# Kernel optimization log

Measured on AMD Instinct MI355X. Metric: run time of the kernel, lower is better.

Reference implementation:

```python
import jax, jax.numpy as jnp
import numpy as np

DIM = 256
NEMB = 1024
NUM = 4
KS = (1, 3, 5, 7)
B, S = 8, 2048


def _conv_same(x, w, b):
    # x: [B,1,S,D], w: [1,1,k,D] -> SAME padding, stride 1 keeps [B,1,S,D]
    y = jax.lax.conv_general_dilated(x, w, window_strides=(1, 1), padding='SAME',
                                     dimension_numbers=('NCHW', 'OIHW', 'NCHW'))
    return jax.nn.relu(y + b[None, :, None, None])


def setup_inputs() -> dict:
    key = jax.random.key(0)
    ks = jax.random.split(key, 12)
    inp = {'x': jax.random.normal(ks[0], (B, S, DIM), jnp.float32)}
    for i, k in enumerate(KS):
        inp[f'conv_w{i}'] = jax.random.normal(ks[1 + i], (1, 1, k, DIM), jnp.float32) * 0.05
        inp[f'conv_b{i}'] = jnp.zeros((1,), jnp.float32)
    inp['embeds'] = jax.random.normal(ks[9], (NUM, DIM, NEMB), jnp.float32)
    inp['gate_w'] = jax.random.normal(ks[10], (NUM, DIM), jnp.float32) * 0.05
    inp['gate_b'] = jnp.zeros((NUM,), jnp.float32)
    return inp


def reference(x, conv_w0, conv_b0, conv_w1, conv_b1, conv_w2, conv_b2,
              conv_w3, conv_b3, embeds, gate_w, gate_b):
    conv_ws = (conv_w0, conv_w1, conv_w2, conv_w3)
    conv_bs = (conv_b0, conv_b1, conv_b2, conv_b3)
    D = x.shape[-1]
    xc = x[:, None]  # [B,1,S,D]
    # per-codebook conv+relu inputs, flattened to tokens: [N, T, D]
    flats = jnp.stack([_conv_same(xc, w, b).reshape(-1, D)
                       for w, b in zip(conv_ws, conv_bs)], axis=0)
    T = flats.shape[1]
    # squared euclidean distance to codebook: [N, T, E]
    x2 = jnp.sum(flats * flats, axis=-1, keepdims=True)
    e2 = jnp.sum(embeds * embeds, axis=1)[:, None, :]
    dist = x2 - 2.0 * jnp.einsum('ntd,nde->nte', flats, embeds) + e2
    ind = jnp.argmin(dist, axis=-1)  # [N, T]
    embT = jnp.swapaxes(embeds, 1, 2)  # [N, E, D]
    quant = jnp.take_along_axis(embT, ind[:, :, None], axis=1)  # [N, T, D]
    # straight-through estimator
    z_q_all = flats + jax.lax.stop_gradient(quant - flats)  # [N, T, D]
    # gated combine (code_mode == 'sum'): gate from first codebook's z_q
    gate_logits = z_q_all[0] @ gate_w.T + gate_b  # [T, N]
    gate = jax.nn.softmax(gate_logits, axis=-1)
    z_q = jnp.einsum('ntd,tn->td', z_q_all, gate)  # [T, D]
    argmin = jnp.swapaxes(ind, 0, 1)  # [T, N] == cat of [T,1] per book
    inputs_cat = jnp.swapaxes(flats, 0, 1).reshape(T, NUM * D)
    quant_cat = jnp.swapaxes(quant, 0, 1).reshape(T, NUM * D)
    return z_q, argmin, inputs_cat, quant_cat
```

## Files before the change

### kernel.cpp

```cpp
#include <hip/hip_runtime.h>
#include <hip/hip_bf16.h>

#define SEQ   2048
#define Dm    256
#define NE    1024
#define TT    16384
#define TAU   0.05f
#define FLAGCAP 131072

typedef __attribute__((ext_vector_type(8))) short          bf16x8;
typedef __attribute__((ext_vector_type(4))) float          f32x4;
typedef __attribute__((ext_vector_type(8))) unsigned short us8;

__device__ __forceinline__ void bfsplit(float x, unsigned short& h, unsigned short& l){
    __hip_bfloat16 bh = __float2bfloat16(x);
    h = *reinterpret_cast<unsigned short*>(&bh);
    union { unsigned u; float f; } c; c.u = (unsigned)h << 16;
    __hip_bfloat16 bl = __float2bfloat16(x - c.f);
    l = *reinterpret_cast<unsigned short*>(&bl);
}

__global__ void k_transpose(const float* __restrict__ emb, float* __restrict__ embT){
    __shared__ float tile[32][33];
    const int n  = blockIdx.z;
    const int e0 = blockIdx.x << 5, d0 = blockIdx.y << 5;
    const int tx = threadIdx.x, ty = threadIdx.y;
    const float* src = emb + (size_t)n * Dm * NE;
    float* dst = embT + (size_t)n * NE * Dm;
    #pragma unroll
    for (int i = ty; i < 32; i += 8)
        tile[i][tx] = src[(size_t)(d0 + i) * NE + e0 + tx];
    __syncthreads();
    #pragma unroll
    for (int i = ty; i < 32; i += 8)
        dst[(size_t)(e0 + i) * Dm + d0 + tx] = tile[tx][i];
}

__global__ void k_e2(const float* __restrict__ emb, float* __restrict__ e2,
                     int* __restrict__ cnt){
    if (blockIdx.x == 0 && blockIdx.y == 0 && threadIdx.x == 0) *cnt = 0;
    const int n = blockIdx.y;
    const int e = (blockIdx.x << 8) + threadIdx.x;
    const float* p = emb + (size_t)n * Dm * NE + e;
    float s = 0.f;
    #pragma unroll 8
    for (int d = 0; d < Dm; ++d){ float v = p[(size_t)d * NE]; s = fmaf(v, v, s); }
    e2[n * NE + e] = s;
}

__global__ __launch_bounds__(256) void k_cvt(const float* __restrict__ embT,
                                             unsigned short* __restrict__ eh,
                                             unsigned short* __restrict__ el){
    const int i = ((blockIdx.x << 8) + threadIdx.x) << 2;
    const float4 v = *reinterpret_cast<const float4*>(&embT[i]);
    ushort4 h, l;
    bfsplit(v.x, h.x, l.x); bfsplit(v.y, h.y, l.y);
    bfsplit(v.z, h.z, l.z); bfsplit(v.w, h.w, l.w);
    *reinterpret_cast<ushort4*>(&eh[i]) = h;
    *reinterpret_cast<ushort4*>(&el[i]) = l;
}

__global__ __launch_bounds__(256) void k_prep(
    const float* __restrict__ w0, const float* __restrict__ w1,
    const float* __restrict__ w2, const float* __restrict__ w3,
    unsigned short* __restrict__ bth, unsigned short* __restrict__ btl)
{
    const int dh = blockIdx.x;
    const int n  = blockIdx.y;
    const int kk = 2 * n + 1;
    if (dh >= kk) return;
    const float* wr[4] = { w0, w1, w2, w3 };
    const float* wp = wr[n] + dh * Dm;
    const int d = threadIdx.x;
    const size_t base = ((size_t)((n * 7 + dh) * 256 + d)) << 8;
    for (int mc = 0; mc < 256; mc += 4){
        ushort4 h, l;
        #pragma unroll
        for (int q = 0; q < 4; ++q){
            const int j = mc + q - d + 127;
            const float v = ((unsigned)j < 256u) ? wp[j] : 0.f;
            unsigned short hh, ll;
            bfsplit(v, hh, ll);
            (&h.x)[q] = hh; (&l.x)[q] = ll;
        }
        *reinterpret_cast<ushort4*>(&bth[base + mc]) = h;
        *reinterpret_cast<ushort4*>(&btl[base + mc]) = l;
    }
}

__global__ __launch_bounds__(256, 2) void k_conv(
    const float* __restrict__ x,
    const unsigned short* __restrict__ bth, const unsigned short* __restrict__ btl,
    const float* __restrict__ b0, const float* __restrict__ b1,
    const float* __restrict__ b2, const float* __restrict__ b3,
    float* __restrict__ ic)
{
    __shared__ alignas(16) unsigned short Ahs[70][264];
    __shared__ alignas(16) unsigned short Als[70][264];

    const int tid  = threadIdx.x;
    const int lane = tid & 63;
    const int w    = tid >> 6;
    const int tx   = lane & 15, tg = lane >> 4;
    const int bx   = blockIdx.x;
    const int n    = bx >> 8;
    const int t0   = (bx & 255) << 6;
    const int bb   = t0 >> 11, s0 = t0 & (SEQ - 1);
    const int kk   = 2 * n + 1, pad = n;
    const int nrows = 64 + 2 * pad;

    for (int idx = tid; idx < (nrows << 6); idx += 256){
        const int r = idx >> 6, c4 = (idx & 63) << 2;
        const int s = s0 - pad + r;
        float4 v = make_float4(0.f, 0.f, 0.f, 0.f);
        if ((unsigned)s < (unsigned)SEQ)
            v = *reinterpret_cast<const float4*>(&x[(size_t)((bb << 11) + s) * Dm + c4]);
        ushort4 h, l;
        bfsplit(v.x, h.x, l.x); bfsplit(v.y, h.y, l.y);
        bfsplit(v.z, h.z, l.z); bfsplit(v.w, h.w, l.w);
        *reinterpret_cast<ushort4*>(&Ahs[r][c4]) = h;
        *reinterpret_cast<ushort4*>(&Als[r][c4]) = l;
    }
    __syncthreads();

    f32x4 acc[4][4];
    #pragma unroll
    for (int rb = 0; rb < 4; ++rb)
        #pragma unroll
        for (int cb = 0; cb < 4; ++cb)
            acc[rb][cb] = f32x4{0.f, 0.f, 0.f, 0.f};

    #pragma unroll 1
    for (int dh = 0; dh < kk; ++dh){
        #pragma unroll
        for (int ks = 0; ks < 8; ++ks){
            const int m0 = ks << 5;
            bf16x8 ah[4], al[4];
            #pragma unroll
            for (int rb = 0; rb < 4; ++rb){
                const int row = (rb << 4) + tx + dh;
                ah[rb] = *reinterpret_cast<const bf16x8*>(&Ahs[row][m0 + (tg << 3)]);
                al[rb] = *reinterpret_cast<const bf16x8*>(&Als[row][m0 + (tg << 3)]);
            }
            #pragma unroll
            for (int cb = 0; cb < 4; ++cb){
                const int d0 = (w << 6) + (cb << 4);
                if (m0 <= d0 + 143 && m0 >= d0 - 158){
                    const size_t gg = ((size_t)((n * 7 + dh) * 256 + d0 + tx) << 8) + m0 + (tg << 3);
                    const bf16x8 bh = *reinterpret_cast<const bf16x8*>(&bth[gg]);
                    const bf16x8 bl = *reinterpret_cast<const bf16x8*>(&btl[gg]);
                    #pragma unroll
                    for (int rb = 0; rb < 4; ++rb){
                        acc[rb][cb] = __builtin_amdgcn_mfma_f32_16x16x32_bf16(ah[rb], bh, acc[rb][cb], 0, 0, 0);
                        acc[rb][cb] = __builtin_amdgcn_mfma_f32_16x16x32_bf16(ah[rb], bl, acc[rb][cb], 0, 0, 0);
                        acc[rb][cb] = __builtin_amdgcn_mfma_f32_16x16x32_bf16(al[rb], bh, acc[rb][cb], 0, 0, 0);
                    }
                }
            }
        }
    }

    const float* bP[4] = { b0, b1, b2, b3 };
    const float bias = bP[n][0];
    #pragma unroll
    for (int rb = 0; rb < 4; ++rb)
        #pragma unroll
        for (int cb = 0; cb < 4; ++cb)
            #pragma unroll
            for (int r = 0; r < 4; ++r){
                const int trow = (rb << 4) + (tg << 2) + r;
                const int d    = (w << 6) + (cb << 4) + tx;
                const float v  = fmaxf(acc[rb][cb][r] + bias, 0.f);
                ic[(size_t)(t0 + trow) * 1024 + (n << 8) + d] = v;
            }
}

#define LOADB(BH, BL, ksv) { \
    _Pragma("unroll") \
    for (int cb = 0; cb < 4; ++cb){ \
        const size_t gg = ebbase[cb] + ((ksv) << 5); \
        BH[cb] = *reinterpret_cast<const bf16x8*>(&ebh[gg]); \
        BL[cb] = *reinterpret_cast<const bf16x8*>(&ebl[gg]); \
    } \
}
#define DOSTEP(BH, BL, ksv) { \
    bf16x8 ah[4], al[4]; \
    _Pragma("unroll") \
    for (int rb = 0; rb < 4; ++rb){ \
        ah[rb] = *reinterpret_cast<const bf16x8*>(&Ahs[(rb << 4) + tx][((ksv) << 5) + (tg << 3)]); \
        al[rb] = *reinterpret_cast<const bf16x8*>(&Als[(rb << 4) + tx][((ksv) << 5) + (tg << 3)]); \
    } \
    _Pragma("unroll") \
    for (int rb = 0; rb < 4; ++rb){ \
        _Pragma("unroll") \
        for (int cb = 0; cb < 4; ++cb){ \
            acc[rb][cb] = __builtin_amdgcn_mfma_f32_16x16x32_bf16(ah[rb], BH[cb], acc[rb][cb], 0, 0, 0); \
            acc[rb][cb] = __builtin_amdgcn_mfma_f32_16x16x32_bf16(ah[rb], BL[cb], acc[rb][cb], 0, 0, 0); \
            acc[rb][cb] = __builtin_amdgcn_mfma_f32_16x16x32_bf16(al[rb], BH[cb], acc[rb][cb], 0, 0, 0); \
        } \
    } \
}

__global__ __launch_bounds__(256, 2) void k_vq(
    const float* __restrict__ ic,
    const unsigned short* __restrict__ ebh, const unsigned short* __restrict__ ebl,
    const float* __restrict__ e2g, int* __restrict__ idx_ws, float* __restrict__ am,
    int* __restrict__ cnt, int2* __restrict__ flags)
{
    __shared__ alignas(16) unsigned short Ahs[64][264];
    __shared__ alignas(16) unsigned short Als[64][264];

    const int tid  = threadIdx.x;
    const int lane = tid & 63;
    const int w    = tid >> 6;
    const int tx   = lane & 15, tg = lane >> 4;
    const int bx   = blockIdx.x;
    const int n    = bx >> 8;
    const int t0   = (bx & 255) << 6;

    #pragma unroll
    for (int i = 0; i < 16; ++i){
        const int idx = tid + (i << 8);
        const int row = idx >> 6, c4 = (idx & 63) << 2;
        const float4 v = *reinterpret_cast<const float4*>(
            &ic[(size_t)(t0 + row) * 1024 + (n << 8) + c4]);
        ushort4 h, l;
        bfsplit(v.x, h.x, l.x); bfsplit(v.y, h.y, l.y);
        bfsplit(v.z, h.z, l.z); bfsplit(v.w, h.w, l.w);
        *reinterpret_cast<ushort4*>(&Ahs[row][c4]) = h;
        *reinterpret_cast<ushort4*>(&Als[row][c4]) = l;
    }
    __syncthreads();

    float mn[16], mn2[16]; int mi[16];
    #pragma unroll
    for (int s = 0; s < 16; ++s){ mn[s] = 3.4e38f; mn2[s] = 3.4e38f; mi[s] = 0; }

    #pragma unroll 1
    for (int ec = 0; ec < 4; ++ec){
        f32x4 acc[4][4];
        #pragma unroll
        for (int rb = 0; rb < 4; ++rb)
            #pragma unroll
            for (int cb = 0; cb < 4; ++cb)
                acc[rb][cb] = f32x4{0.f, 0.f, 0.f, 0.f};

        size_t ebbase[4];
        #pragma unroll
        for (int cb = 0; cb < 4; ++cb){
            const int e = (w << 8) + (ec << 6) + (cb << 4) + tx;
            ebbase[cb] = ((size_t)((n << 10) + e) << 8) + (tg << 3);
        }

        bf16x8 bh0[4], bl0[4], bh1[4], bl1[4];
        LOADB(bh0, bl0, 0);
        #pragma unroll
        for (int kp = 0; kp < 4; ++kp){
            LOADB(bh1, bl1, 2 * kp + 1);
            DOSTEP(bh0, bl0, 2 * kp);
            if (kp < 3) LOADB(bh0, bl0, 2 * kp + 2);
            DOSTEP(bh1, bl1, 2 * kp + 1);
        }

        #pragma unroll
        for (int cb = 0; cb < 4; ++cb){
            const int e = (w << 8) + (ec << 6) + (cb << 4) + tx;
            const float ee = e2g[(n << 10) + e];
            #pragma unroll
            for (int rb = 0; rb < 4; ++rb)
                #pragma unroll
                for (int r = 0; r < 4; ++r){
                    const float v = fmaf(-2.f, acc[rb][cb][r], ee);
                    const int s = (rb << 2) + r;
                    if (v < mn[s]){ mn2[s] = mn[s]; mn[s] = v; mi[s] = e; }
                    else if (v < mn2[s]){ mn2[s] = v; }
                }
        }
    }

    #pragma unroll
    for (int sft = 1; sft < 16; sft <<= 1){
        #pragma unroll
        for (int s = 0; s < 16; ++s){
            const float om  = __shfl_xor(mn[s],  sft, 64);
            const float om2 = __shfl_xor(mn2[s], sft, 64);
            const int   oi  = __shfl_xor(mi[s],  sft, 64);
            if (om < mn[s] || (om == mn[s] && oi < mi[s])){
                mn2[s] = fminf(mn[s], om2);
                mn[s] = om; mi[s] = oi;
            } else {
                mn2[s] = fminf(mn2[s], om);
            }
        }
    }
    __syncthreads();
    float* redMn  = reinterpret_cast<float*>(&Ahs[0][0]);
    float* redMn2 = redMn + 256;
    int*   redMi  = reinterpret_cast<int*>(redMn + 512);
    if (tx == 0){
        #pragma unroll
        for (int rb = 0; rb < 4; ++rb)
            #pragma unroll
            for (int r = 0; r < 4; ++r){
                const int row = (rb << 4) + (tg << 2) + r;
                const int s = (rb << 2) + r;
                redMn [(w << 6) + row] = mn[s];
                redMn2[(w << 6) + row] = mn2[s];
                redMi [(w << 6) + row] = mi[s];
            }
    }
    __syncthreads();
    if (tid < 64){
        const int row = tid;
        float bmn = redMn[row], bmn2 = redMn2[row];
        int   bmi = redMi[row];
        #pragma unroll
        for (int wv = 1; wv < 4; ++wv){
            const float om  = redMn [(wv << 6) + row];
            const float om2 = redMn2[(wv << 6) + row];
            const int   oi  = redMi [(wv << 6) + row];
            if (om < bmn || (om == bmn && oi < bmi)){
                bmn2 = fminf(bmn, om2);
                bmn = om; bmi = oi;
            } else {
                bmn2 = fminf(bmn2, om);
            }
        }
        const int t = t0 + row;
        idx_ws[t * 4 + n] = bmi;
        am[(size_t)t * 4 + n] = (float)bmi;
        if (bmn2 - bmn < TAU){
            const int pos = atomicAdd(cnt, 1);
            if (pos < FLAGCAP) flags[pos] = make_int2(t, n);
        }
    }
}

__global__ __launch_bounds__(256) void k_fix(
    const float* __restrict__ x,
    const float* __restrict__ w0, const float* __restrict__ w1,
    const float* __restrict__ w2, const float* __restrict__ w3,
    const float* __restrict__ b0, const float* __restrict__ b1,
    const float* __restrict__ b2, const float* __restrict__ b3,
    const float* __restrict__ embT,
    const int* __restrict__ cnt, const int2* __restrict__ flags,
    int* __restrict__ idx_ws, float* __restrict__ am)
{
    __shared__ double fl[Dm];
    __shared__ double rD[4];
    __shared__ int    rE[4];
    const int tid = threadIdx.x;
    const int total = (*cnt < FLAGCAP) ? *cnt : FLAGCAP;
    const float* wP[4] = { w0, w1, w2, w3 };
    const float* bP[4] = { b0, b1, b2, b3 };
    const int   kN[4] = { 1, 3, 5, 7 };

    for (int item = blockIdx.x; item < total; item += gridDim.x){
        const int2 f = flags[item];
        const int t = f.x, n = f.y;
        const int bb = t >> 11, s = t & (SEQ - 1);
        const int k = kN[n], pad = (k - 1) >> 1;
        {
            const int d = tid;
            double acc = (double)bP[n][0];
            for (int dh = 0; dh < k; ++dh){
                const int sr = s - pad + dh;
                if ((unsigned)sr < (unsigned)SEQ){
                    const float* xr = x + (size_t)((bb << 11) + sr) * Dm;
                    const float* wr = wP[n] + dh * Dm;
                    const int lo = (d - 127 < 0) ? 0 : d - 127;
                    const int hi = (d + 129 > Dm) ? Dm : d + 129;
                    for (int m = lo; m < hi; ++m)
                        acc += (double)xr[m] * (double)wr[m - d + 127];
                }
            }
            fl[d] = (acc > 0.0) ? acc : 0.0;
        }
        __syncthreads();
        double bD = 1e300; int bE = 0;
        #pragma unroll
        for (int ee = 0; ee < 4; ++ee){
            const int e = (ee << 8) + tid;
            const float* ep = embT + ((size_t)n * NE + e) * Dm;
            double dot = 0.0, e2 = 0.0;
            for (int d = 0; d < Dm; ++d){
                const double v = (double)ep[d];
                dot += v * fl[d];
                e2  += v * v;
            }
            const double dist = e2 - 2.0 * dot;
            if (dist < bD || (dist == bD && e < bE)){ bD = dist; bE = e; }
        }
        #pragma unroll
        for (int sft = 1; sft < 64; sft <<= 1){
            const double od = __shfl_xor(bD, sft, 64);
            const int    oe = __shfl_xor(bE, sft, 64);
            if (od < bD || (od == bD && oe < bE)){ bD = od; bE = oe; }
        }
        if ((tid & 63) == 0){ rD[tid >> 6] = bD; rE[tid >> 6] = bE; }
        __syncthreads();
        if (tid == 0){
            #pragma unroll
            for (int wv = 1; wv < 4; ++wv)
                if (rD[wv] < rD[0] || (rD[wv] == rD[0] && rE[wv] < rE[0])){
                    rD[0] = rD[wv]; rE[0] = rE[wv];
                }
            idx_ws[t * 4 + n] = rE[0];
            am[(size_t)t * 4 + n] = (float)rE[0];
        }
        __syncthreads();
    }
}

__global__ __launch_bounds__(256) void k_final(
    const int* __restrict__ idx_ws, const float* __restrict__ embT,
    const float* __restrict__ gw, const float* __restrict__ gb,
    float* __restrict__ qc, float* __restrict__ zq)
{
    __shared__ float gws[4][Dm];
    const int tid = threadIdx.x;
    for (int i = tid; i < 4 * Dm; i += 256) gws[i >> 8][i & 255] = gw[i];
    __syncthreads();
    const int t = (blockIdx.x << 2) + (tid >> 6);
    const int lane = tid & 63, d0 = lane << 2;

    float q[4][4];
    #pragma unroll
    for (int n = 0; n < 4; ++n){
        const int e = idx_ws[t * 4 + n];
        const float4 v = *reinterpret_cast<const float4*>(
            &embT[((size_t)n * NE + e) * Dm + d0]);
        q[n][0] = v.x; q[n][1] = v.y; q[n][2] = v.z; q[n][3] = v.w;
        *reinterpret_cast<float4*>(&qc[(size_t)t * 1024 + n * Dm + d0]) = v;
    }
    float part[4];
    #pragma unroll
    for (int n = 0; n < 4; ++n){
        part[n] = q[0][0] * gws[n][d0]     + q[0][1] * gws[n][d0 + 1]
                + q[0][2] * gws[n][d0 + 2] + q[0][3] * gws[n][d0 + 3];
    }
    #pragma unroll
    for (int s = 1; s < 64; s <<= 1){
        #pragma unroll
        for (int n = 0; n < 4; ++n) part[n] += __shfl_xor(part[n], s, 64);
    }
    float lg[4];
    #pragma unroll
    for (int n = 0; n < 4; ++n) lg[n] = part[n] + gb[n];
    const float mx = fmaxf(fmaxf(lg[0], lg[1]), fmaxf(lg[2], lg[3]));
    float ex[4], ssum = 0.f;
    #pragma unroll
    for (int n = 0; n < 4; ++n){ ex[n] = expf(lg[n] - mx); ssum += ex[n]; }
    const float inv = 1.f / ssum;
    float z[4];
    #pragma unroll
    for (int dd = 0; dd < 4; ++dd)
        z[dd] = (ex[0] * q[0][dd] + ex[1] * q[1][dd] + ex[2] * q[2][dd] + ex[3] * q[3][dd]) * inv;
    *reinterpret_cast<float4*>(&zq[(size_t)t * Dm + d0]) =
        make_float4(z[0], z[1], z[2], z[3]);
}

extern "C" void kernel_launch(void* const* d_in, const int* in_sizes, int n_in,
                              void* d_out, int out_size, void* d_ws, size_t ws_size,
                              hipStream_t stream)
{
    const float* x   = (const float*)d_in[0];
    const float* w0  = (const float*)d_in[1];
    const float* b0  = (const float*)d_in[2];
    const float* w1  = (const float*)d_in[3];
    const float* b1  = (const float*)d_in[4];
    const float* w2  = (const float*)d_in[5];
    const float* b2  = (const float*)d_in[6];
    const float* w3  = (const float*)d_in[7];
    const float* b3  = (const float*)d_in[8];
    const float* emb = (const float*)d_in[9];
    const float* gw  = (const float*)d_in[10];
    const float* gb  = (const float*)d_in[11];

    float* out = (float*)d_out;
    float* zq = out;
    float* am = out + 4194304;
    float* ic = out + 4259840;
    float* qc = out + 21037056;

    float* ws    = (float*)d_ws;
    float* embT  = ws;
    float* e2    = ws + 1048576;
    int*   idxs  = (int*)(ws + 1052672);
    int*   cnt   = (int*)(ws + 1118208);
    int2*  flags = (int2*)(ws + 1118212);
    unsigned short* ebh = (unsigned short*)(ws + 1380360);
    unsigned short* ebl = (unsigned short*)(ws + 1904648);
    unsigned short* bth = (unsigned short*)(ws + 2428936);
    unsigned short* btl = (unsigned short*)(ws + 3346440);

    hipLaunchKernelGGL(k_transpose, dim3(32, 8, 4), dim3(32, 8), 0, stream, emb, embT);
    hipLaunchKernelGGL(k_e2,        dim3(4, 4),     dim3(256),   0, stream, emb, e2, cnt);
    hipLaunchKernelGGL(k_cvt,       dim3(1024),     dim3(256),   0, stream, embT, ebh, ebl);
    hipLaunchKernelGGL(k_prep,      dim3(7, 4),     dim3(256),   0, stream,
                       w0, w1, w2, w3, bth, btl);
    hipLaunchKernelGGL(k_conv,      dim3(1024),     dim3(256),   0, stream,
                       x, bth, btl, b0, b1, b2, b3, ic);
    hipLaunchKernelGGL(k_vq,        dim3(1024),     dim3(256),   0, stream,
                       ic, ebh, ebl, e2, idxs, am, cnt, flags);
    hipLaunchKernelGGL(k_fix,       dim3(512),      dim3(256),   0, stream,
                       x, w0, w1, w2, w3, b0, b1, b2, b3, embT, cnt, flags, idxs, am);
    hipLaunchKernelGGL(k_final,     dim3(4096),     dim3(256),   0, stream,
                       idxs, embT, gw, gb, qc, zq);
}
```

Baseline: 675.7 us.

## Pre-split conv output to bf16, tighten tie threshold, and speed up the fix kernel

The conv kernel now also writes bf16 hi/lo splits of its output into the not-yet-written quant_cat region of the output buffer. k_vq loads these directly instead of re-reading fp32 and splitting it. The near-tie threshold TAU drops from 0.05 to 0.02, so fewer tokens are sent to the exact double-precision fix pass. k_fix stages the x window in shared memory, uses float4 codebook loads with split accumulators, and launches on a larger grid. The lower threshold risks missing near-ties that the approximate bf16x3 distance gets wrong, and the extra split writes add write traffic in the conv kernel.

Result: faster. 626.1 us (-7.3%).

```diff
diff --git a/kernel.cpp b/kernel.cpp
--- a/kernel.cpp
+++ b/kernel.cpp
@@ -5,7 +5,7 @@
 #define Dm    256
 #define NE    1024
 #define TT    16384
-#define TAU   0.05f
+#define TAU   0.02f
 #define FLAGCAP 131072
 
 typedef __attribute__((ext_vector_type(8))) short          bf16x8;
@@ -93,7 +93,8 @@
     const unsigned short* __restrict__ bth, const unsigned short* __restrict__ btl,
     const float* __restrict__ b0, const float* __restrict__ b1,
     const float* __restrict__ b2, const float* __restrict__ b3,
-    float* __restrict__ ic)
+    float* __restrict__ ic,
+    unsigned short* __restrict__ ich, unsigned short* __restrict__ icl)
 {
     __shared__ alignas(16) unsigned short Ahs[70][264];
     __shared__ alignas(16) unsigned short Als[70][264];
@@ -171,7 +172,11 @@
                 const int trow = (rb << 4) + (tg << 2) + r;
                 const int d    = (w << 6) + (cb << 4) + tx;
                 const float v  = fmaxf(acc[rb][cb][r] + bias, 0.f);
-                ic[(size_t)(t0 + trow) * 1024 + (n << 8) + d] = v;
+                const size_t oidx = (size_t)(t0 + trow) * 1024 + (n << 8) + d;
+                ic[oidx] = v;
+                unsigned short hh, ll;
+                bfsplit(v, hh, ll);
+                ich[oidx] = hh; icl[oidx] = ll;
             }
 }
 
@@ -202,7 +207,7 @@
 }
 
 __global__ __launch_bounds__(256, 2) void k_vq(
-    const float* __restrict__ ic,
+    const unsigned short* __restrict__ ich, const unsigned short* __restrict__ icl,
     const unsigned short* __restrict__ ebh, const unsigned short* __restrict__ ebl,
     const float* __restrict__ e2g, int* __restrict__ idx_ws, float* __restrict__ am,
     int* __restrict__ cnt, int2* __restrict__ flags)
@@ -219,16 +224,12 @@
     const int t0   = (bx & 255) << 6;
 
     #pragma unroll
-    for (int i = 0; i < 16; ++i){
+    for (int i = 0; i < 8; ++i){
         const int idx = tid + (i << 8);
-        const int row = idx >> 6, c4 = (idx & 63) << 2;
-        const float4 v = *reinterpret_cast<const float4*>(
-            &ic[(size_t)(t0 + row) * 1024 + (n << 8) + c4]);
-        ushort4 h, l;
-        bfsplit(v.x, h.x, l.x); bfsplit(v.y, h.y, l.y);
-        bfsplit(v.z, h.z, l.z); bfsplit(v.w, h.w, l.w);
-        *reinterpret_cast<ushort4*>(&Ahs[row][c4]) = h;
-        *reinterpret_cast<ushort4*>(&Als[row][c4]) = l;
+        const int row = idx >> 5, ch = (idx & 31) << 3;
+        const size_t g = (size_t)(t0 + row) * 1024 + (n << 8) + ch;
+        *reinterpret_cast<us8*>(&Ahs[row][ch]) = *reinterpret_cast<const us8*>(&ich[g]);
+        *reinterpret_cast<us8*>(&Als[row][ch]) = *reinterpret_cast<const us8*>(&icl[g]);
     }
     __syncthreads();
 
@@ -346,49 +347,66 @@
     const int* __restrict__ cnt, const int2* __restrict__ flags,
     int* __restrict__ idx_ws, float* __restrict__ am)
 {
+    __shared__ double xs[7][Dm];
     __shared__ double fl[Dm];
     __shared__ double rD[4];
     __shared__ int    rE[4];
     const int tid = threadIdx.x;
+    const int lane = tid & 63, w = tid >> 6;
     const int total = (*cnt < FLAGCAP) ? *cnt : FLAGCAP;
     const float* wP[4] = { w0, w1, w2, w3 };
     const float* bP[4] = { b0, b1, b2, b3 };
-    const int   kN[4] = { 1, 3, 5, 7 };
 
     for (int item = blockIdx.x; item < total; item += gridDim.x){
         const int2 f = flags[item];
         const int t = f.x, n = f.y;
         const int bb = t >> 11, s = t & (SEQ - 1);
-        const int k = kN[n], pad = (k - 1) >> 1;
+        const int k = 2 * n + 1, pad = n;
+        for (int idx = tid; idx < (k << 8); idx += 256){
+            const int r = idx >> 8, m = idx & 255;
+            const int sr = s - pad + r;
+            xs[r][m] = ((unsigned)sr < (unsigned)SEQ)
+                       ? (double)x[(size_t)((bb << 11) + sr) * Dm + m] : 0.0;
+        }
+        __syncthreads();
         {
             const int d = tid;
-            double acc = (double)bP[n][0];
+            double a0 = (double)bP[n][0], a1 = 0.0;
             for (int dh = 0; dh < k; ++dh){
-                const int sr = s - pad + dh;
-                if ((unsigned)sr < (unsigned)SEQ){
-                    const float* xr = x + (size_t)((bb << 11) + sr) * Dm;
-                    const float* wr = wP[n] + dh * Dm;
-                    const int lo = (d - 127 < 0) ? 0 : d - 127;
-                    const int hi = (d + 129 > Dm) ? Dm : d + 129;
-                    for (int m = lo; m < hi; ++m)
-                        acc += (double)xr[m] * (double)wr[m - d + 127];
+                const float* wr = wP[n] + dh * Dm;
+                const int lo = (d - 127 < 0) ? 0 : d - 127;
+                const int hi = (d + 129 > Dm) ? Dm : d + 129;
+                int m = lo;
+                for (; m + 1 < hi; m += 2){
+                    a0 += xs[dh][m]     * (double)wr[m - d + 127];
+                    a1 += xs[dh][m + 1] * (double)wr[m - d + 128];
                 }
-            }
+                if (m < hi) a0 += xs[dh][m] * (double)wr[m - d + 127];
+            }
+            const double acc = a0 + a1;
             fl[d] = (acc > 0.0) ? acc : 0.0;
         }
         __syncthreads();
         double bD = 1e300; int bE = 0;
-        #pragma unroll
-        for (int ee = 0; ee < 4; ++ee){
-            const int e = (ee << 8) + tid;
-            const float* ep = embT + ((size_t)n * NE + e) * Dm;
-            double dot = 0.0, e2 = 0.0;
-            for (int d = 0; d < Dm; ++d){
-                const double v = (double)ep[d];
-                dot += v * fl[d];
-                e2  += v * v;
-            }
-            const double dist = e2 - 2.0 * dot;
+        const float* ebase = embT + (size_t)n * NE * Dm;
+        #pragma unroll 1
+        for (int p = 0; p < 4; ++p){
+            const int e = (p << 8) + tid;
+            const float4* row = reinterpret_cast<const float4*>(&ebase[(size_t)e * Dm]);
+            double d0 = 0.0, d1 = 0.0, s0 = 0.0, s1 = 0.0;
+            for (int j = 0; j < 64; j += 2){
+                const float4 va = row[j], vb = row[j + 1];
+                const int m = j << 2;
+                d0 += (double)va.x * fl[m]     + (double)va.y * fl[m + 1]
+                    + (double)va.z * fl[m + 2] + (double)va.w * fl[m + 3];
+                s0 += (double)va.x * (double)va.x + (double)va.y * (double)va.y
+                    + (double)va.z * (double)va.z + (double)va.w * (double)va.w;
+                d1 += (double)vb.x * fl[m + 4] + (double)vb.y * fl[m + 5]
+                    + (double)vb.z * fl[m + 6] + (double)vb.w * fl[m + 7];
+                s1 += (double)vb.x * (double)vb.x + (double)vb.y * (double)vb.y
+                    + (double)vb.z * (double)vb.z + (double)vb.w * (double)vb.w;
+            }
+            const double dist = (s0 + s1) - 2.0 * (d0 + d1);
             if (dist < bD || (dist == bD && e < bE)){ bD = dist; bE = e; }
         }
         #pragma unroll
@@ -397,7 +415,7 @@
             const int    oe = __shfl_xor(bE, sft, 64);
             if (od < bD || (od == bD && oe < bE)){ bD = od; bE = oe; }
         }
-        if ((tid & 63) == 0){ rD[tid >> 6] = bD; rE[tid >> 6] = bE; }
+        if (lane == 0){ rD[w] = bD; rE[w] = bE; }
         __syncthreads();
         if (tid == 0){
             #pragma unroll
@@ -482,6 +500,8 @@
     float* am = out + 4194304;
     float* ic = out + 4259840;
     float* qc = out + 21037056;
+    unsigned short* ich = (unsigned short*)qc;
+    unsigned short* icl = ich + 16777216;
 
     float* ws    = (float*)d_ws;
     float* embT  = ws;
@@ -500,10 +520,10 @@
     hipLaunchKernelGGL(k_prep,      dim3(7, 4),     dim3(256),   0, stream,
                        w0, w1, w2, w3, bth, btl);
     hipLaunchKernelGGL(k_conv,      dim3(1024),     dim3(256),   0, stream,
-                       x, bth, btl, b0, b1, b2, b3, ic);
+                       x, bth, btl, b0, b1, b2, b3, ic, ich, icl);
     hipLaunchKernelGGL(k_vq,        dim3(1024),     dim3(256),   0, stream,
-                       ic, ebh, ebl, e2, idxs, am, cnt, flags);
-    hipLaunchKernelGGL(k_fix,       dim3(512),      dim3(256),   0, stream,
+                       ich, icl, ebh, ebl, e2, idxs, am, cnt, flags);
+    hipLaunchKernelGGL(k_fix,       dim3(2048),     dim3(256),   0, stream,
                        x, w0, w1, w2, w3, b0, b1, b2, b3, embT, cnt, flags, idxs, am);
     hipLaunchKernelGGL(k_final,     dim3(4096),     dim3(256),   0, stream,
                        idxs, embT, gw, gb, qc, zq);
```
